# Optimization experiments

Measured on AMD Instinct MI355X. Metric: run time of the kernel, lower is better.

Reference implementation:

```python
import jax, jax.numpy as jnp
import numpy as np

H = 16
ROPE_BASE = 10000.0

def _rope_cos_sin(seq_len, d_k, dtype):
    inv_freq = 1.0 / (ROPE_BASE ** (jnp.arange(0, d_k, 2, dtype=jnp.float32) / d_k))
    t = jnp.arange(seq_len, dtype=jnp.float32)
    freqs = jnp.einsum('s,d->sd', t, inv_freq)          # [S, d_k/2]
    emb = jnp.concatenate([freqs, freqs], axis=-1)       # [S, d_k]
    return jnp.cos(emb).astype(dtype), jnp.sin(emb).astype(dtype)

def _rotate_half(x):
    x1, x2 = jnp.split(x, 2, axis=-1)
    return jnp.concatenate([-x2, x1], axis=-1)

def setup_inputs() -> dict:
    key = jax.random.key(0)
    ks = jax.random.split(key, 11)
    B, S, D = 2, 2048, 1024
    sc = 0.02
    return {
        'query': jax.random.normal(ks[0], (B, S, D), jnp.float32),
        'key':   jax.random.normal(ks[1], (B, S, D), jnp.float32),
        'value': jax.random.normal(ks[2], (B, S, D), jnp.float32),
        'Wq': jax.random.normal(ks[3], (D, D), jnp.float32) * sc,
        'bq': jnp.zeros((D,), jnp.float32),
        'Wk': jax.random.normal(ks[4], (D, D), jnp.float32) * sc,
        'bk': jnp.zeros((D,), jnp.float32),
        'Wv': jax.random.normal(ks[5], (D, D), jnp.float32) * sc,
        'bv': jnp.zeros((D,), jnp.float32),
        'Wo': jax.random.normal(ks[6], (D, D), jnp.float32) * sc,
        'bo': jnp.zeros((D,), jnp.float32),
    }

def reference(query, key, value, Wq, bq, Wk, bk, Wv, bv, Wo, bo):
    B, S, D = query.shape
    d_k = D // H
    # QKV projections (torch Linear: x @ W.T + b), split heads -> [B, H, S, d_k]
    def proj(x, W, b):
        return (x @ W.T + b).reshape(B, S, H, d_k).transpose(0, 2, 1, 3)
    q = proj(query, Wq, bq)
    k = proj(key, Wk, bk)
    v = proj(value, Wv, bv)
    # Rotary position embedding applied to q and k
    cos, sin = _rope_cos_sin(S, d_k, q.dtype)            # [S, d_k]
    cos = cos[None, None, :, :]
    sin = sin[None, None, :, :]
    q = q * cos + _rotate_half(q) * sin
    k = k * cos + _rotate_half(k) * sin
    # Scaled dot-product attention
    scores = jnp.einsum('bhqd,bhkd->bhqk', q, k) / jnp.sqrt(jnp.asarray(d_k, q.dtype))
    attn = jax.nn.softmax(scores, axis=-1)
    x = jnp.einsum('bhqk,bhkd->bhqd', attn, v)           # [B, H, S, d_k]
    x = x.transpose(0, 2, 1, 3).reshape(B, S, D)
    return x @ Wo.T + bo
```

## Files before the change

kernel.cpp:

```cpp
#include <hip/hip_runtime.h>
#include <hip/hip_bf16.h>
#include <math.h>


#define B_ 2
#define S_ 2048
#define D_ 1024
#define H_ 16
#define DK 64

typedef __attribute__((ext_vector_type(8)))  __bf16    bf16x8;
typedef __attribute__((ext_vector_type(8)))  _Float16  f16x8;
typedef __attribute__((ext_vector_type(4)))  float     f32x4;
typedef __attribute__((ext_vector_type(16))) float     f32x16;
typedef __attribute__((ext_vector_type(8)))  unsigned short u16x8;
typedef __attribute__((ext_vector_type(4)))  unsigned short u16x4;

#if __has_builtin(__builtin_amdgcn_exp2f)
#define EXP2(x) __builtin_amdgcn_exp2f(x)
#else
#define EXP2(x) exp2f(x)
#endif

static __device__ __forceinline__ unsigned short f2bf(float x) {
    union { float f; unsigned u; } v; v.f = x;
    unsigned r = v.u + 0x7FFFu + ((v.u >> 16) & 1u);
    return (unsigned short)(r >> 16);
}
static __device__ __forceinline__ unsigned cvtpk(float lo, float hi) {
    unsigned r;
    asm("v_cvt_pk_bf16_f32 %0, %1, %2" : "=v"(r) : "v"(lo), "v"(hi));
    return r;
}
static __device__ __forceinline__ unsigned cvtpk16(float lo, float hi) {
    unsigned r;
    asm("v_cvt_pkrtz_f16_f32 %0, %1, %2" : "=v"(r) : "v"(lo), "v"(hi));
    return r;
}
static __device__ __forceinline__ void gload_lds16(const void* g, void* l) {
    __builtin_amdgcn_global_load_lds(
        (const __attribute__((address_space(1))) void*)g,
        (__attribute__((address_space(3))) void*)l, 16, 0, 0);
}
static __device__ __forceinline__ int swz(int R, int c) {
    return ((R >> 1) << 6) + (((((R & 1) << 2) | c) ^ ((R >> 1) & 7)) << 3);
}
union ffrag  { unsigned u[4]; f16x8  v; };
static __device__ __forceinline__ void splitpk16(float e0, float e1,
                                                 unsigned& hd, unsigned& ld) {
    hd = cvtpk16(e0, e1);
    union { unsigned u; _Float16 h[2]; } t; t.u = hd;
    ld = cvtpk16(e0 - (float)t.h[0], e1 - (float)t.h[1]);
}

__global__ __launch_bounds__(256) void wsplit4(
    const float* __restrict__ W0, const float* __restrict__ W1,
    const float* __restrict__ W2, const float* __restrict__ W3,
    unsigned short* __restrict__ out)
{
    const int idx = blockIdx.x * 256 + threadIdx.x;
    const int t = idx >> 17;
    const size_t e = (size_t)(idx & 131071) * 8;
    const float* src = (t==0 ? W0 : t==1 ? W1 : t==2 ? W2 : W3) + e;
    float4 a = *(const float4*)src;
    float4 b = *(const float4*)(src + 4);
    float x[8] = {a.x,a.y,a.z,a.w,b.x,b.y,b.z,b.w};
    union { _Float16 h[8]; u16x8 v; } Hh;
    #pragma unroll
    for (int j = 0; j < 8; ++j) Hh.h[j] = (_Float16)x[j];
    *(u16x8*)(out + (size_t)t * 1048576 + e) = Hh.v;
}

__global__ __launch_bounds__(512) void trigemm(
    const float* __restrict__ Aq, const float* __restrict__ Ak,
    const float* __restrict__ Av, const unsigned short* __restrict__ wsp,
    const float* __restrict__ bq, const float* __restrict__ bk,
    const float* __restrict__ bv,
    unsigned short* __restrict__ qb, unsigned short* __restrict__ kb,
    unsigned short* __restrict__ vt)
{
    __shared__ __align__(16) char ldsb[32768];
    const int pid = blockIdx.z;
    const float* A    = (pid==0) ? Aq : (pid==1) ? Ak : Av;
    const float* bias = (pid==0) ? bq : (pid==1) ? bk : bv;
    const unsigned short* Whp = wsp + (size_t)pid * 1048576;

    const int tid = threadIdx.x;
    const int w = tid >> 6, lane = tid & 63;
    const int l15 = lane & 15, g4 = lane >> 4;
    const int wr = w >> 1, wc = w & 1;
    const int bx = blockIdx.x, by = blockIdx.y;

    const int arow = tid >> 2, ac = tid & 3;
    const float* gpA = A + (size_t)(bx*128 + arow) * 1024 + ac * 8;
    const int aoff = swz(arow, ac);

    const int sr_ = tid >> 3, slot_ = tid & 7;
    const int z_  = slot_ ^ (sr_ & 7);
    const int wR_ = sr_*2 + (z_ >> 2);
    const unsigned short* gpW = Whp + (size_t)(by*128 + wR_) * 1024 + (z_ & 3) * 8;

    f32x4 acc[2][4];
    #pragma unroll
    for (int m = 0; m < 2; ++m)
        #pragma unroll
        for (int n = 0; n < 4; ++n) acc[m][n] = (f32x4){0.f,0.f,0.f,0.f};

    {
        float4 p0 = *(const float4*)(gpA);
        float4 p1 = *(const float4*)(gpA + 4);
        gload_lds16(gpW, ldsb + 8192 + tid * 16);
        union { unsigned u[4]; u16x8 v; } hh;
        hh.u[0] = cvtpk16(p0.x, p0.y); hh.u[1] = cvtpk16(p0.z, p0.w);
        hh.u[2] = cvtpk16(p1.x, p1.y); hh.u[3] = cvtpk16(p1.z, p1.w);
        *(u16x8*)((unsigned short*)ldsb + aoff) = hh.v;
    }
    asm volatile("s_waitcnt vmcnt(0) lgkmcnt(0)" ::: "memory");
    __builtin_amdgcn_s_barrier();
    asm volatile("" ::: "memory");

    for (int t = 0; t < 32; ++t) {
        const int cur = t & 1;
        float4 n0, n1;
        if (t < 31) {
            n0 = *(const float4*)(gpA + (t+1)*32);
            n1 = *(const float4*)(gpA + (t+1)*32 + 4);
            gload_lds16(gpW + (size_t)(t+1)*32, ldsb + (cur^1)*16384 + 8192 + tid*16);
            asm volatile("s_waitcnt vmcnt(3)" ::: "memory");
        } else {
            asm volatile("s_waitcnt vmcnt(0)" ::: "memory");
        }
        __builtin_amdgcn_s_barrier();
        asm volatile("" ::: "memory");

        const unsigned short* Ab = (const unsigned short*)(ldsb + cur*16384);
        const unsigned short* Wb = Ab + 4096;
        f16x8 ah[2], wh4[4];
        #pragma unroll
        for (int m = 0; m < 2; ++m)
            ah[m] = *(const f16x8*)(Ab + swz(wr*32 + m*16 + l15, g4));
        #pragma unroll
        for (int n = 0; n < 4; ++n)
            wh4[n] = *(const f16x8*)(Wb + swz(wc*64 + n*16 + l15, g4));
        #pragma unroll
        for (int m = 0; m < 2; ++m)
            #pragma unroll
            for (int n = 0; n < 4; ++n)
                acc[m][n] = __builtin_amdgcn_mfma_f32_16x16x32_f16(ah[m], wh4[n], acc[m][n], 0,0,0);

        if (t < 31) {
            union { unsigned u[4]; u16x8 v; } hh;
            hh.u[0] = cvtpk16(n0.x, n0.y); hh.u[1] = cvtpk16(n0.z, n0.w);
            hh.u[2] = cvtpk16(n1.x, n1.y); hh.u[3] = cvtpk16(n1.z, n1.w);
            *(u16x8*)((unsigned short*)(ldsb + (cur^1)*16384) + aoff) = hh.v;
        }
        asm volatile("s_waitcnt lgkmcnt(0)" ::: "memory");
        __builtin_amdgcn_s_barrier();
        asm volatile("" ::: "memory");
    }

    const int colBase = by*128 + wc*64;
    const int rowBase = bx*128 + wr*32;
    const int h = colBase >> 6;

    if (pid < 2) {
        unsigned short* Out = pid ? kb : qb;
        const float QSC = pid ? 1.0f : 0.125f * 1.44269504088896340736f;
        #pragma unroll
        for (int m = 0; m < 2; ++m) {
            const int srow0 = rowBase + m*16 + g4*4;
            const int b = srow0 >> 11;
            unsigned short* hb2 = Out + (size_t)(b*H_ + h) * S_ * DK;
            #pragma unroll
            for (int n = 0; n < 2; ++n) {
                const int d = n*16 + l15;
                const float invf = exp2f((float)d * -0.4152410118609203f);
                const float b1 = bias[h*64 + d], b2 = bias[h*64 + d + 32];
                #pragma unroll
                for (int r = 0; r < 4; ++r) {
                    const int s = (srow0 + r) & 2047;
                    const float x1 = acc[m][n][r]   + b1;
                    const float x2 = acc[m][n+2][r] + b2;
                    float sn, cc;
                    __sincosf((float)s * invf, &sn, &cc);
                    const float o1 = (x1*cc - x2*sn) * QSC;
                    const float o2 = (x2*cc + x1*sn) * QSC;
                    if (pid == 0) {
                        unsigned short* dst = hb2 + (size_t)s * DK;
                        dst[d]      = f2bf(o1);
                        dst[d + 32] = f2bf(o2);
                    } else {
                        unsigned short* tb = hb2 + (s >> 6) * 4096 + (s & 63) * 8;
                        tb[(d >> 3) * 512 + (d & 7)]        = f2bf(o1);
                        tb[(d >> 3) * 512 + 2048 + (d & 7)] = f2bf(o2);
                    }
                }
            }
        }
    } else {
        #pragma unroll
        for (int m = 0; m < 2; ++m) {
            const int srow0 = rowBase + m*16 + g4*4;
            const int b = srow0 >> 11, s0 = srow0 & 2047;
            unsigned short* tb = vt + (size_t)(b*H_ + h) * S_ * DK
                               + (s0 >> 6) * 4096 + ((s0 & 63) >> 3) * 512 + (s0 & 7);
            #pragma unroll
            for (int n = 0; n < 4; ++n) {
                const int d = n*16 + l15;
                const float bb = bias[h*64 + d];
                u16x4 pk;
                #pragma unroll
                for (int r = 0; r < 4; ++r) pk[r] = f2bf(acc[m][n][r] + bb);
                *(u16x4*)(tb + d * 8) = pk;
            }
        }
    }
}

__global__ __launch_bounds__(512) void mfma_gemm0(
    const unsigned short* __restrict__ Ah, const unsigned short* __restrict__ Al,
    const unsigned short* __restrict__ Wh,
    const float* __restrict__ bias, float* __restrict__ Out)
{
    __shared__ __align__(16) char ldsb[49152];
    const int tid = threadIdx.x;
    const int w = tid >> 6, lane = tid & 63;
    const int l15 = lane & 15, g4 = lane >> 4;
    const int wr = w >> 1, wc = w & 1;
    const int bx = blockIdx.x, by = blockIdx.y;

    const int u_ = w >> 1, qq = w & 1;
    const unsigned short* gsrc = (u_==0) ? Ah : (u_==1) ? Al : Wh;
    const int row0 = (u_ < 2) ? bx * 128 : by * 128;
    const int lr8 = lane >> 3;
    const int zz  = (lane & 7) ^ lr8;
    const int wR0 = qq*64 + (lr8 << 1) + (zz >> 2);
    const unsigned short* gp0 = gsrc + (size_t)(row0 + wR0) * 1024 + (zz & 3) * 8;

    f32x4 acc[2][4];
    #pragma unroll
    for (int m = 0; m < 2; ++m)
        #pragma unroll
        for (int n = 0; n < 4; ++n) acc[m][n] = (f32x4){0.f,0.f,0.f,0.f};

    #define STAGE(T, BUF) do {                                              \
        if (w < 6) {                                                        \
            const unsigned short* g_ = gp0 + (size_t)(T) * 32;              \
            char* d_ = ldsb + (BUF)*24576 + u_*8192 + qq*4096;              \
            gload_lds16(g_,          d_);                                   \
            gload_lds16(g_ + 16384,  d_ + 1024);                            \
            gload_lds16(g_ + 32768,  d_ + 2048);                            \
            gload_lds16(g_ + 49152,  d_ + 3072);                            \
        }                                                                   \
    } while (0)

    STAGE(0, 0);
    asm volatile("s_waitcnt vmcnt(0)" ::: "memory");
    __builtin_amdgcn_s_barrier();
    asm volatile("" ::: "memory");

    for (int t = 0; t < 32; ++t) {
        const int cur = t & 1;
        if (t < 31) {
            STAGE(t + 1, cur ^ 1);
            asm volatile("s_waitcnt vmcnt(4)" ::: "memory");
        } else {
            asm volatile("s_waitcnt vmcnt(0)" ::: "memory");
        }
        __builtin_amdgcn_s_barrier();
        asm volatile("" ::: "memory");

        const unsigned short* Ahb = (const unsigned short*)(ldsb + cur*24576);
        const unsigned short* Alb = Ahb + 4096;
        const unsigned short* Whb = Ahb + 8192;

        f16x8 ah2[2], al2[2], wh4[4];
        #pragma unroll
        for (int m = 0; m < 2; ++m) {
            const int off = swz(wr*32 + m*16 + l15, g4);
            ah2[m] = *(const f16x8*)(Ahb + off);
            al2[m] = *(const f16x8*)(Alb + off);
        }
        #pragma unroll
        for (int n = 0; n < 4; ++n) {
            const int off = swz(wc*64 + n*16 + l15, g4);
            wh4[n] = *(const f16x8*)(Whb + off);
        }
        #pragma unroll
        for (int m = 0; m < 2; ++m)
            #pragma unroll
            for (int n = 0; n < 4; ++n) {
                acc[m][n] = __builtin_amdgcn_mfma_f32_16x16x32_f16(ah2[m], wh4[n], acc[m][n], 0,0,0);
                acc[m][n] = __builtin_amdgcn_mfma_f32_16x16x32_f16(al2[m], wh4[n], acc[m][n], 0,0,0);
            }

        asm volatile("" ::: "memory");
        __builtin_amdgcn_s_barrier();
        asm volatile("" ::: "memory");
    }
    #undef STAGE

    const int colBase = by*128 + wc*64;
    const int rowBase = bx*128 + wr*32;
    #pragma unroll
    for (int m = 0; m < 2; ++m) {
        const int row = rowBase + m*16 + g4*4;
        #pragma unroll
        for (int n = 0; n < 4; ++n) {
            const int col = colBase + n*16 + l15;
            const float bb = bias[col];
            #pragma unroll
            for (int r = 0; r < 4; ++r)
                Out[(size_t)(row + r) * 1024 + col] = acc[m][n][r] + bb;
        }
    }
}

__global__ __launch_bounds__(512, 1) void attn_mfma8(
    const unsigned short* __restrict__ Qb, const unsigned short* __restrict__ Kb,
    const unsigned short* __restrict__ Vt,
    unsigned short* __restrict__ Xh, unsigned short* __restrict__ Xl)
{
    __shared__ __align__(16) char lds[65536];
    const unsigned bid = blockIdx.x;
    const int xcd = bid & 7, idx = bid >> 3;
    const int bh  = xcd * 4 + (idx >> 3);
    const int qt  = idx & 7;
    const int tid = threadIdx.x;
    const int w = tid >> 6, lane = tid & 63;
    const int l31 = lane & 31, hi = lane >> 5;
    const size_t bhO = (size_t)bh * S_ * DK;
    const int q0 = qt * 256 + w * 32;

    const int u0   = w * 4;
    const int isV  = u0 >> 4;
    const int u15  = u0 & 15;
    const int su0  = u15 >> 3;
    const unsigned short* sb = (isV ? Vt : Kb) + bhO;
    const int ch0 = u15 & 7;
    char* const dbase = lds;

    bf16x8 qf[4];
    #pragma unroll
    for (int ks = 0; ks < 4; ++ks)
        qf[ks] = *(const bf16x8*)(Qb + bhO + (size_t)(q0 + l31) * DK + ks*16 + hi*8);

    f32x16 oT[2];
    #pragma unroll
    for (int dh = 0; dh < 2; ++dh)
        #pragma unroll
        for (int r = 0; r < 16; ++r) oT[dh][r] = 0.f;
    float l_ = 0.f;

    #define ASTAGE(T, BUF) do {                                                     \
        const unsigned short* g_ = sb + (size_t)((T)*2 + su0) * 4096 + ch0 * 512    \
                                   + lane * 8;                                      \
        char* d_ = dbase + (BUF)*32768 + isV*16384 + su0*8192 + ch0*1024 + lane*16; \
        gload_lds16(g_,         d_);                                                \
        gload_lds16(g_ + 512,   d_ + 1024);                                         \
        gload_lds16(g_ + 1024,  d_ + 2048);                                         \
        gload_lds16(g_ + 1536,  d_ + 3072);                                         \
    } while (0)

    ASTAGE(0, 0);
    asm volatile("s_waitcnt vmcnt(0)" ::: "memory");
    __builtin_amdgcn_s_barrier();
    asm volatile("" ::: "memory");

    for (int t = 0; t < 16; ++t) {
        const int cur = t & 1;
        if (t < 15) {
            ASTAGE(t + 1, cur ^ 1);
            asm volatile("s_waitcnt vmcnt(4)" ::: "memory");
        } else {
            asm volatile("s_waitcnt vmcnt(0)" ::: "memory");
        }
        __builtin_amdgcn_s_barrier();
        asm volatile("" ::: "memory");

        const char* Kl = lds + cur * 32768;
        const char* Vl = Kl + 16384;

        f32x16 s2[4];
        __builtin_amdgcn_s_setprio(1);
        #pragma unroll
        for (int kb2 = 0; kb2 < 4; ++kb2) {
            f32x16 a;
            #pragma unroll
            for (int r = 0; r < 16; ++r) a[r] = 0.f;
            const char* kbase = Kl + (kb2 >> 1) * 8192 + ((kb2 & 1) * 32 + l31) * 16;
            #pragma unroll
            for (int ks = 0; ks < 4; ++ks) {
                bf16x8 kf = *(const bf16x8*)(kbase + (ks*2 + hi) * 1024);
                a = __builtin_amdgcn_mfma_f32_32x32x16_bf16(kf, qf[ks], a, 0, 0, 0);
            }
            s2[kb2] = a;
        }
        __builtin_amdgcn_s_setprio(0);

        {
            float lsum = 0.f;
            #pragma unroll
            for (int kb2 = 0; kb2 < 4; ++kb2)
                #pragma unroll
                for (int r = 0; r < 16; ++r) {
                    const float p = EXP2(s2[kb2][r]);
                    s2[kb2][r] = p; lsum += p;
                }
            l_ += lsum;
        }

        #pragma unroll
        for (int ks2 = 0; ks2 < 8; ++ks2) {
            const int kb2 = ks2 >> 1;
            const int R0  = (ks2 & 1) * 8;
            unsigned a0 = cvtpk(s2[kb2][R0+0], s2[kb2][R0+1]);
            unsigned a1 = cvtpk(s2[kb2][R0+2], s2[kb2][R0+3]);
            unsigned b0 = cvtpk(s2[kb2][R0+4], s2[kb2][R0+5]);
            unsigned b1 = cvtpk(s2[kb2][R0+6], s2[kb2][R0+7]);
            asm("v_permlane32_swap_b32 %0, %1" : "+v"(a0), "+v"(b0));
            asm("v_permlane32_swap_b32 %0, %1" : "+v"(a1), "+v"(b1));
            union { unsigned u[4]; bf16x8 v; } pf;
            pf.u[0] = a0; pf.u[1] = a1; pf.u[2] = b0; pf.u[3] = b1;
            const char* vbase = Vl + (ks2 >> 2) * 8192 + (((ks2 & 3) * 2) + hi) * 1024;
            __builtin_amdgcn_s_setprio(1);
            #pragma unroll
            for (int dh = 0; dh < 2; ++dh) {
                bf16x8 vf = *(const bf16x8*)(vbase + (dh*32 + l31) * 16);
                oT[dh] = __builtin_amdgcn_mfma_f32_32x32x16_bf16(vf, pf.v, oT[dh], 0, 0, 0);
            }
            __builtin_amdgcn_s_setprio(0);
        }

        asm volatile("" ::: "memory");
        __builtin_amdgcn_s_barrier();
        asm volatile("" ::: "memory");
    }
    #undef ASTAGE

    l_ += __shfl_xor(l_, 32, 64);
    const float inv = 1.0f / l_;
    const int b = bh >> 4, h = bh & 15;
    const int q = q0 + l31;
    unsigned short* xh = Xh + (((size_t)b * S_ + q) * H_ + h) * DK;
    unsigned short* xl = Xl + (((size_t)b * S_ + q) * H_ + h) * DK;
    #pragma unroll
    for (int dh = 0; dh < 2; ++dh)
        #pragma unroll
        for (int tt = 0; tt < 4; ++tt) {
            const int dk0 = dh*32 + tt*8 + hi*4;
            const float o0 = oT[dh][tt*4 + 0] * inv;
            const float o1 = oT[dh][tt*4 + 1] * inv;
            const float o2 = oT[dh][tt*4 + 2] * inv;
            const float o3 = oT[dh][tt*4 + 3] * inv;
            union { unsigned u[2]; u16x4 v; } hv, lv;
            splitpk16(o0, o1, hv.u[0], lv.u[0]);
            splitpk16(o2, o3, hv.u[1], lv.u[1]);
            *(u16x4*)(xh + dk0) = hv.v;
            *(u16x4*)(xl + dk0) = lv.v;
        }
}

extern "C" void kernel_launch(void* const* d_in, const int* in_sizes, int n_in,
                              void* d_out, int out_size, void* d_ws, size_t ws_size,
                              hipStream_t stream)
{
    const float* query = (const float*)d_in[0];
    const float* key   = (const float*)d_in[1];
    const float* value = (const float*)d_in[2];
    const float* Wq = (const float*)d_in[3];  const float* bq = (const float*)d_in[4];
    const float* Wk = (const float*)d_in[5];  const float* bk = (const float*)d_in[6];
    const float* Wv = (const float*)d_in[7];  const float* bv = (const float*)d_in[8];
    const float* Wo = (const float*)d_in[9];  const float* bo = (const float*)d_in[10];
    float* out = (float*)d_out;

    char* ws = (char*)d_ws;
    const size_t MB = (size_t)1 << 20;
    unsigned short* Xh  = (unsigned short*)(ws + 0*MB);
    unsigned short* Xl  = (unsigned short*)(ws + 8*MB);
    unsigned short* qb  = (unsigned short*)(ws + 16*MB);
    unsigned short* vt  = (unsigned short*)(ws + 24*MB);
    unsigned short* kb  = (unsigned short*)(ws + 40*MB);
    unsigned short* wsp = (unsigned short*)(ws + 48*MB);
    unsigned short* Woh = wsp + 3145728;

    wsplit4<<<2048, 256, 0, stream>>>(Wq, Wk, Wv, Wo, wsp);

    trigemm<<<dim3(32, 8, 3), 512, 0, stream>>>(query, key, value, wsp,
                                                bq, bk, bv, qb, kb, vt);

    attn_mfma8<<<256, 512, 0, stream>>>(qb, kb, vt, Xh, Xl);

    mfma_gemm0<<<dim3(32, 8), 512, 0, stream>>>(Xh, Xl, Woh, bo, out);
}
```

Measured before the change: 117.9 us.

## Merge double barriers into one per iteration and prefetch A two tiles ahead

In the projection, output-GEMM and attention loops, each iteration now issues its next-stage async copies and waits once at the end, so the two barriers per iteration become one. The QKV projection GEMM also prefetches fp32 A rows two tiles ahead using register ping-pong through a lambda unrolled by two, which gives the global loads more time to land. The aim is to cut barrier stalls and hide load latency. The cost is more live registers, and there is a risk of an LDS write-after-read race if a wave refills a buffer that another wave is still reading.

```diff
diff --git a/kernel.cpp b/kernel.cpp
--- a/kernel.cpp
+++ b/kernel.cpp
@@ -45,7 +45,6 @@
 static __device__ __forceinline__ int swz(int R, int c) {
     return ((R >> 1) << 6) + (((((R & 1) << 2) | c) ^ ((R >> 1) & 7)) << 3);
 }
-union ffrag  { unsigned u[4]; f16x8  v; };
 static __device__ __forceinline__ void splitpk16(float e0, float e1,
                                                  unsigned& hd, unsigned& ld) {
     hd = cvtpk16(e0, e1);
@@ -106,33 +105,33 @@
         #pragma unroll
         for (int n = 0; n < 4; ++n) acc[m][n] = (f32x4){0.f,0.f,0.f,0.f};
 
+    float4 pa0, pa1, pb0, pb1;
+
     {
-        float4 p0 = *(const float4*)(gpA);
-        float4 p1 = *(const float4*)(gpA + 4);
         gload_lds16(gpW, ldsb + 8192 + tid * 16);
+        pa0 = *(const float4*)(gpA);
+        pa1 = *(const float4*)(gpA + 4);
+        asm volatile("s_waitcnt vmcnt(0)" ::: "memory");
         union { unsigned u[4]; u16x8 v; } hh;
-        hh.u[0] = cvtpk16(p0.x, p0.y); hh.u[1] = cvtpk16(p0.z, p0.w);
-        hh.u[2] = cvtpk16(p1.x, p1.y); hh.u[3] = cvtpk16(p1.z, p1.w);
+        hh.u[0] = cvtpk16(pa0.x, pa0.y); hh.u[1] = cvtpk16(pa0.z, pa0.w);
+        hh.u[2] = cvtpk16(pa1.x, pa1.y); hh.u[3] = cvtpk16(pa1.z, pa1.w);
         *(u16x8*)((unsigned short*)ldsb + aoff) = hh.v;
-    }
-    asm volatile("s_waitcnt vmcnt(0) lgkmcnt(0)" ::: "memory");
-    __builtin_amdgcn_s_barrier();
-    asm volatile("" ::: "memory");
-
-    for (int t = 0; t < 32; ++t) {
-        const int cur = t & 1;
-        float4 n0, n1;
-        if (t < 31) {
-            n0 = *(const float4*)(gpA + (t+1)*32);
-            n1 = *(const float4*)(gpA + (t+1)*32 + 4);
-            gload_lds16(gpW + (size_t)(t+1)*32, ldsb + (cur^1)*16384 + 8192 + tid*16);
-            asm volatile("s_waitcnt vmcnt(3)" ::: "memory");
-        } else {
-            asm volatile("s_waitcnt vmcnt(0)" ::: "memory");
-        }
+        pa0 = *(const float4*)(gpA + 32);
+        pa1 = *(const float4*)(gpA + 32 + 4);
+        asm volatile("s_waitcnt lgkmcnt(0)" ::: "memory");
         __builtin_amdgcn_s_barrier();
         asm volatile("" ::: "memory");
-
+    }
+
+    auto body = [&](int t, float4& ca0, float4& ca1, float4& cb0, float4& cb1) {
+        const int cur = t & 1;
+        if (t < 31)
+            gload_lds16(gpW + (size_t)(t+1)*32,
+                        ldsb + (cur^1)*16384 + 8192 + tid*16);
+        if (t < 30) {
+            cb0 = *(const float4*)(gpA + (size_t)(t+2)*32);
+            cb1 = *(const float4*)(gpA + (size_t)(t+2)*32 + 4);
+        }
         const unsigned short* Ab = (const unsigned short*)(ldsb + cur*16384);
         const unsigned short* Wb = Ab + 4096;
         f16x8 ah[2], wh4[4];
@@ -150,13 +149,20 @@
 
         if (t < 31) {
             union { unsigned u[4]; u16x8 v; } hh;
-            hh.u[0] = cvtpk16(n0.x, n0.y); hh.u[1] = cvtpk16(n0.z, n0.w);
-            hh.u[2] = cvtpk16(n1.x, n1.y); hh.u[3] = cvtpk16(n1.z, n1.w);
+            hh.u[0] = cvtpk16(ca0.x, ca0.y); hh.u[1] = cvtpk16(ca0.z, ca0.w);
+            hh.u[2] = cvtpk16(ca1.x, ca1.y); hh.u[3] = cvtpk16(ca1.z, ca1.w);
             *(u16x8*)((unsigned short*)(ldsb + (cur^1)*16384) + aoff) = hh.v;
-        }
-        asm volatile("s_waitcnt lgkmcnt(0)" ::: "memory");
-        __builtin_amdgcn_s_barrier();
-        asm volatile("" ::: "memory");
+            if (t < 30)
+                asm volatile("s_waitcnt vmcnt(2) lgkmcnt(0)" ::: "memory");
+            else
+                asm volatile("s_waitcnt vmcnt(0) lgkmcnt(0)" ::: "memory");
+            __builtin_amdgcn_s_barrier();
+            asm volatile("" ::: "memory");
+        }
+    };
+    for (int t2 = 0; t2 < 32; t2 += 2) {
+        body(t2,     pa0, pa1, pb0, pb1);
+        body(t2 + 1, pb0, pb1, pa0, pa1);
     }
 
     const int colBase = by*128 + wc*64;
@@ -261,14 +267,7 @@
 
     for (int t = 0; t < 32; ++t) {
         const int cur = t & 1;
-        if (t < 31) {
-            STAGE(t + 1, cur ^ 1);
-            asm volatile("s_waitcnt vmcnt(4)" ::: "memory");
-        } else {
-            asm volatile("s_waitcnt vmcnt(0)" ::: "memory");
-        }
-        __builtin_amdgcn_s_barrier();
-        asm volatile("" ::: "memory");
+        if (t < 31) STAGE(t + 1, cur ^ 1);
 
         const unsigned short* Ahb = (const unsigned short*)(ldsb + cur*24576);
         const unsigned short* Alb = Ahb + 4096;
@@ -294,9 +293,11 @@
                 acc[m][n] = __builtin_amdgcn_mfma_f32_16x16x32_f16(al2[m], wh4[n], acc[m][n], 0,0,0);
             }
 
-        asm volatile("" ::: "memory");
-        __builtin_amdgcn_s_barrier();
-        asm volatile("" ::: "memory");
+        if (t < 31) {
+            asm volatile("s_waitcnt vmcnt(0)" ::: "memory");
+            __builtin_amdgcn_s_barrier();
+            asm volatile("" ::: "memory");
+        }
     }
     #undef STAGE
 
@@ -369,14 +370,7 @@
 
     for (int t = 0; t < 16; ++t) {
         const int cur = t & 1;
-        if (t < 15) {
-            ASTAGE(t + 1, cur ^ 1);
-            asm volatile("s_waitcnt vmcnt(4)" ::: "memory");
-        } else {
-            asm volatile("s_waitcnt vmcnt(0)" ::: "memory");
-        }
-        __builtin_amdgcn_s_barrier();
-        asm volatile("" ::: "memory");
+        if (t < 15) ASTAGE(t + 1, cur ^ 1);
 
         const char* Kl = lds + cur * 32768;
         const char* Vl = Kl + 16384;
@@ -432,9 +426,11 @@
             __builtin_amdgcn_s_setprio(0);
         }
 
-        asm volatile("" ::: "memory");
-        __builtin_amdgcn_s_barrier();
-        asm volatile("" ::: "memory");
+        if (t < 15) {
+            asm volatile("s_waitcnt vmcnt(0)" ::: "memory");
+            __builtin_amdgcn_s_barrier();
+            asm volatile("" ::: "memory");
+        }
     }
     #undef ASTAGE
 
```

New measurement: 127.2 us. 1.08x slower.
